# Kernel tuning notes

Hardware: AMD Instinct MI355X
Metric: run time of the kernel (lower is better)

Reference implementation:

```python
import jax, jax.numpy as jnp
import numpy as np

L, EMB, NH, HD, V = 4, 1024, 16, 64, 16000
Q, B, M = 512, 4, 512


def layer_norm(x, g, b, eps=1e-5):
    mu = jnp.mean(x, -1, keepdims=True)
    var = jnp.mean((x - mu) ** 2, -1, keepdims=True)
    return (x - mu) * jax.lax.rsqrt(var + eps) * g + b


def rel_shift(x):
    # x: [q, i, b, h] -> Transformer-XL relative shift via zero-pad + reshape
    q, i, bb, h = x.shape
    zp = jnp.zeros((q, 1, bb, h), x.dtype)
    return jnp.concatenate([zp, x], axis=1).reshape(i + 1, q, bb, h)[1:].reshape(q, i, bb, h)


def setup_inputs() -> dict:
    key = jax.random.key(0)
    ks = jax.random.split(key, 12)
    s = 0.02
    return {
        'input_idxs': jax.random.randint(ks[0], (Q, B), 0, V, dtype=jnp.int32),
        'memory': jax.random.normal(ks[1], (L, M, B, EMB), jnp.float32),
        'embedding': jax.random.normal(ks[2], (V, EMB), jnp.float32) * s,
        'proj_b': jnp.zeros((V,), jnp.float32),
        'u_bias': jax.random.normal(ks[3], (NH, HD), jnp.float32) * s,
        'v_bias': jax.random.normal(ks[4], (NH, HD), jnp.float32) * s,
        'Wq': jax.random.normal(ks[5], (L, NH * HD, EMB), jnp.float32) * s,
        'Wkv': jax.random.normal(ks[6], (L, 2 * NH * HD, EMB), jnp.float32) * s,
        'Wp': jax.random.normal(ks[7], (L, NH * HD, EMB), jnp.float32) * s,
        'fc_w': jax.random.normal(ks[8], (L, EMB, NH * HD), jnp.float32) * s,
        'ff1_w': jax.random.normal(ks[9], (L, 4 * EMB, EMB), jnp.float32) * s,
        'ff1_b': jnp.zeros((L, 4 * EMB), jnp.float32),
        'ff2_w': jax.random.normal(ks[10], (L, EMB, 4 * EMB), jnp.float32) * s,
        'ff2_b': jnp.zeros((L, EMB), jnp.float32),
        'ln_g': jnp.ones((L, EMB), jnp.float32),
        'ln_b': jnp.zeros((L, EMB), jnp.float32),
    }


def reference(input_idxs, memory, embedding, proj_b, u_bias, v_bias, Wq, Wkv, Wp,
              fc_w, ff1_w, ff1_b, ff2_w, ff2_b, ln_g, ln_b):
    # NOTE: faithful to the source, which uses scale = 1 / head_dim**5 (not **0.5)
    scale = 1.0 / (HD ** 5)
    x = embedding[input_idxs] * jnp.asarray(EMB ** 0.5, jnp.float32)  # [Q,B,E]

    # sinusoidal relative positions, descending M+Q-1 .. 0
    pos = jnp.arange(M + Q - 1, -1, -1, dtype=jnp.float32)
    inv_freq = 1.0 / (10000.0 ** (jnp.arange(0, EMB, 2, dtype=jnp.float32) / EMB))
    angle = pos[:, None] * inv_freq[None, :]
    emb_pos = jnp.concatenate([jnp.sin(angle), jnp.cos(angle)], axis=1)  # [M+Q,E]

    mask = jnp.triu(jnp.ones((Q, M + Q), bool), k=1 + M)  # [Q,I]

    for l in range(L):
        e = jnp.concatenate([memory[l], x], axis=0)  # [I,B,E], I = M+Q
        kv = jnp.einsum('ibe,fe->ibf', e, Wkv[l])
        k, v = jnp.split(kv, 2, axis=-1)
        k = k.reshape(M + Q, B, NH, HD)
        v = v.reshape(M + Q, B, NH, HD)
        q = jnp.einsum('qbe,fe->qbf', x, Wq[l]).reshape(Q, B, NH, HD)
        p = (emb_pos @ Wp[l].T).reshape(M + Q, NH, HD)

        att_c = jnp.einsum('qbhd,ibhd->qibh', q + u_bias, k)
        att_p = rel_shift(jnp.einsum('qbhd,ihd->qibh', q + v_bias, p))
        att = att_c + att_p
        att = jnp.where(mask[:, :, None, None], -jnp.inf, att)
        att = jax.nn.softmax(att * scale, axis=1)

        o = jnp.einsum('qibh,ibhd->qbhd', att, v).reshape(Q, B, NH * HD)
        o = o @ fc_w[l].T
        h = layer_norm(o + x, ln_g[l], ln_b[l])
        f = jax.nn.relu(h @ ff1_w[l].T + ff1_b[l]) @ ff2_w[l].T + ff2_b[l]
        x = layer_norm(f + h, ln_g[l], ln_b[l])

    return x @ embedding.T + proj_b  # tied projection, [Q,B,V]
```

## Files before the change

kernel.cpp:

```cpp
#include <hip/hip_runtime.h>


typedef unsigned short u16;
typedef unsigned int u32;
typedef __bf16 bf16x8 __attribute__((ext_vector_type(8)));
typedef float f32x4 __attribute__((ext_vector_type(4)));

#define AS1 __attribute__((address_space(1)))
#define AS3 __attribute__((address_space(3)))

__device__ __forceinline__ u16 f2bf(float f) {
  u32 u = __float_as_uint(f);
  u32 r = (u + 0x7FFFu + ((u >> 16) & 1u)) >> 16;
  return (u16)r;
}
__device__ __forceinline__ float bf2f(u16 u) {
  return __uint_as_float(((u32)u) << 16);
}

struct alignas(8) us4 { u16 x, y, z, w; };

__global__ void k_conv(const float* __restrict__ src, u16* __restrict__ dst, int n4) {
  int i = blockIdx.x * blockDim.x + threadIdx.x;
  int stride = gridDim.x * blockDim.x;
  const float4* s4 = (const float4*)src;
  us4* d4 = (us4*)dst;
  for (; i < n4; i += stride) {
    float4 v = s4[i];
    us4 o; o.x = f2bf(v.x); o.y = f2bf(v.y); o.z = f2bf(v.z); o.w = f2bf(v.w);
    d4[i] = o;
  }
}

__global__ void k_embed(const int* __restrict__ idx, const float* __restrict__ emb,
                        float* __restrict__ x, u16* __restrict__ xb) {
  int r = blockIdx.x, t = threadIdx.x;
  int id = idx[r];
  float4 v = ((const float4*)(emb + (size_t)id * 1024))[t];
  v.x *= 32.0f; v.y *= 32.0f; v.z *= 32.0f; v.w *= 32.0f;
  ((float4*)(x + (size_t)r * 1024))[t] = v;
  us4 o; o.x = f2bf(v.x); o.y = f2bf(v.y); o.z = f2bf(v.z); o.w = f2bf(v.w);
  ((us4*)(xb + (size_t)r * 1024))[t] = o;
}

__global__ void k_ln(const float* __restrict__ a, const float* __restrict__ res,
                     const float* __restrict__ g, const float* __restrict__ bb,
                     float* __restrict__ outf, u16* __restrict__ outb) {
  int r = blockIdx.x, t = threadIdx.x;
  float4 va = ((const float4*)(a + (size_t)r * 1024))[t];
  float4 vr = ((const float4*)(res + (size_t)r * 1024))[t];
  float y0 = va.x + vr.x, y1 = va.y + vr.y, y2 = va.z + vr.z, y3 = va.w + vr.w;
  float s = y0 + y1 + y2 + y3;
  float sq = y0 * y0 + y1 * y1 + y2 * y2 + y3 * y3;
  for (int o = 32; o > 0; o >>= 1) { s += __shfl_xor(s, o); sq += __shfl_xor(sq, o); }
  __shared__ float ls[8];
  int w = t >> 6;
  if ((t & 63) == 0) { ls[w * 2] = s; ls[w * 2 + 1] = sq; }
  __syncthreads();
  s = ls[0] + ls[2] + ls[4] + ls[6];
  sq = ls[1] + ls[3] + ls[5] + ls[7];
  float mu = s * (1.0f / 1024.0f);
  float var = sq * (1.0f / 1024.0f) - mu * mu;
  float rs = rsqrtf(var + 1e-5f);
  float4 vg = ((const float4*)g)[t];
  float4 vb = ((const float4*)bb)[t];
  float o0 = (y0 - mu) * rs * vg.x + vb.x;
  float o1 = (y1 - mu) * rs * vg.y + vb.y;
  float o2v = (y2 - mu) * rs * vg.z + vb.z;
  float o3 = (y3 - mu) * rs * vg.w + vb.w;
  float4 of; of.x = o0; of.y = o1; of.z = o2v; of.w = o3;
  ((float4*)(outf + (size_t)r * 1024))[t] = of;
  us4 oo; oo.x = f2bf(o0); oo.y = f2bf(o1); oo.z = f2bf(o2v); oo.w = f2bf(o3);
  ((us4*)(outb + (size_t)r * 1024))[t] = oo;
}

__global__ void k_psum(const u16* __restrict__ v, float* __restrict__ part) {
  int bx = blockIdx.x;
  int c = bx >> 4, b = (bx >> 2) & 3, fg = bx & 3;
  int f = fg * 256 + threadIdx.x;
  float s = 0.f;
  for (int j = 0; j < 64; j++) {
    int i = c * 64 + j;
    s += bf2f(v[((size_t)(i * 4 + b)) * 1024 + f]);
  }
  part[(size_t)(c * 4 + b) * 1024 + f] = s;
}

__global__ void k_pmean(const u16* __restrict__ v, const float* __restrict__ part,
                        u16* __restrict__ ob) {
  int bx = blockIdx.x;
  int qc = bx >> 4, b = (bx >> 2) & 3, fg = bx & 3;
  int f = fg * 256 + threadIdx.x;
  float run = 0.f;
  int cend = 8 + qc;
  for (int c = 0; c < cend; c++) run += part[(size_t)(c * 4 + b) * 1024 + f];
  for (int j = 0; j < 64; j++) {
    int i = 512 + qc * 64 + j;
    run += bf2f(v[((size_t)(i * 4 + b)) * 1024 + f]);
    ob[((size_t)((i - 512) * 4 + b)) * 1024 + f] = f2bf(run / (float)(i + 1));
  }
}

template <int BIAS, int RELU, int OUTBF>
__global__ __launch_bounds__(256, 2) void k_gemm(
    const u16* __restrict__ A, const u16* __restrict__ A2, int split,
    const u16* __restrict__ B, float* __restrict__ Cf, u16* __restrict__ Cb,
    const float* __restrict__ bias, int M, int N, int K) {
  __shared__ __align__(16) u16 As[128 * 64];
  __shared__ __align__(16) u16 Bs[128 * 64];
  const int tid = threadIdx.x;
  const int lane = tid & 63, wid = tid >> 6;
  const int la = lane & 15, lb = lane >> 4;
  const int row0 = blockIdx.x * 128, col0 = blockIdx.y * 128;
  const int wm = wid >> 1, wn = wid & 1;
  const size_t Kb = (size_t)K * 2;
  const u16* Au = A; int arow = row0;
  if (row0 >= split) { Au = A2; arow = row0 - split; }
  const char* Ab = (const char*)Au + (size_t)arow * Kb;
  const char* Bb = (const char*)B + (size_t)col0 * Kb;
  f32x4 acc[4][4] = {};
  for (int k0 = 0; k0 < K; k0 += 64) {
#pragma unroll
    for (int s = 0; s < 4; s++) {
      int off = s * 4096 + tid * 16;
      int rr = off >> 7, cb = off & 127;
      __builtin_amdgcn_global_load_lds(
          (AS1 void*)(Ab + (size_t)rr * Kb + (size_t)(k0 * 2 + cb)),
          (AS3 void*)((char*)As + s * 4096 + wid * 1024), 16, 0, 0);
    }
#pragma unroll
    for (int s = 0; s < 4; s++) {
      int off = s * 4096 + tid * 16;
      int rr = off >> 7, cb = off & 127;
      __builtin_amdgcn_global_load_lds(
          (AS1 void*)(Bb + (size_t)rr * Kb + (size_t)(k0 * 2 + cb)),
          (AS3 void*)((char*)Bs + s * 4096 + wid * 1024), 16, 0, 0);
    }
    __syncthreads();
    bf16x8 af[2][4], bfv[2][4];
#pragma unroll
    for (int kk = 0; kk < 2; kk++) {
#pragma unroll
      for (int i = 0; i < 4; i++) {
        af[kk][i] = *reinterpret_cast<const bf16x8*>(
            &As[(wm * 64 + i * 16 + la) * 64 + kk * 32 + lb * 8]);
        bfv[kk][i] = *reinterpret_cast<const bf16x8*>(
            &Bs[(wn * 64 + i * 16 + la) * 64 + kk * 32 + lb * 8]);
      }
    }
#pragma unroll
    for (int kk = 0; kk < 2; kk++)
#pragma unroll
      for (int mi = 0; mi < 4; mi++)
#pragma unroll
        for (int ni = 0; ni < 4; ni++)
          acc[mi][ni] = __builtin_amdgcn_mfma_f32_16x16x32_bf16(
              af[kk][mi], bfv[kk][ni], acc[mi][ni], 0, 0, 0);
    __syncthreads();
  }
#pragma unroll
  for (int ni = 0; ni < 4; ni++) {
    int c = col0 + wn * 64 + ni * 16 + la;
    float bv = 0.f;
    if (BIAS) bv = bias[c];
#pragma unroll
    for (int mi = 0; mi < 4; mi++) {
#pragma unroll
      for (int j = 0; j < 4; j++) {
        int rr = row0 + wm * 64 + mi * 16 + lb * 4 + j;
        float vv = acc[mi][ni][j];
        if (BIAS) vv += bv;
        if (RELU) vv = fmaxf(vv, 0.f);
        if (OUTBF) Cb[(size_t)rr * N + c] = f2bf(vv);
        else       Cf[(size_t)rr * N + c] = vv;
      }
    }
  }
}

extern "C" void kernel_launch(void* const* d_in, const int* in_sizes, int n_in,
                              void* d_out, int out_size, void* d_ws, size_t ws_size,
                              hipStream_t stream) {
  const int* idxs = (const int*)d_in[0];
  const float* memory = (const float*)d_in[1];
  const float* embedding = (const float*)d_in[2];
  const float* proj_b = (const float*)d_in[3];
  const float* Wkv = (const float*)d_in[7];
  const float* fc_w = (const float*)d_in[9];
  const float* ff1_w = (const float*)d_in[10];
  const float* ff1_b = (const float*)d_in[11];
  const float* ff2_w = (const float*)d_in[12];
  const float* ff2_b = (const float*)d_in[13];
  const float* ln_g = (const float*)d_in[14];
  const float* ln_b = (const float*)d_in[15];
  float* out = (float*)d_out;

  float* ws = (float*)d_ws;
  float* x    = ws + 0;
  float* h    = ws + 2097152;
  float* o2   = ws + 4194304;
  u16* xb     = (u16*)(ws + 6291456);
  u16* hb     = (u16*)(ws + 7340032);
  u16* ob     = (u16*)(ws + 8388608);
  float* part = ws + 9437184;
  u16* wvv    = (u16*)(ws + 9502720);
  u16* wfc    = (u16*)(ws + 10027008);
  u16* wf1    = (u16*)(ws + 10551296);
  u16* wf2    = (u16*)(ws + 12648448);
  float* big  = ws + 14745600;
  u16* vbuf   = (u16*)(big);
  u16* memb   = (u16*)(big + 2097152);
  u16* f1     = (u16*)(big + 3145728);
  u16* embb   = (u16*)(big);

  auto conv = [&](const float* s, u16* d, int n) {
    int n4 = n >> 2;
    int blocks = (n4 + 255) / 256; if (blocks > 4096) blocks = 4096;
    k_conv<<<blocks, 256, 0, stream>>>(s, d, n4);
  };

  const int BIG = 1 << 30;
  k_embed<<<2048, 256, 0, stream>>>(idxs, embedding, x, xb);

  for (int l = 0; l < 4; l++) {
    conv(Wkv + (size_t)l * 2097152 + 1048576, wvv, 1048576);
    conv(fc_w + (size_t)l * 1048576, wfc, 1048576);
    conv(ff1_w + (size_t)l * 4194304, wf1, 4194304);
    conv(ff2_w + (size_t)l * 4194304, wf2, 4194304);
    conv(memory + (size_t)l * 2097152, memb, 2097152);

    k_gemm<0, 0, 1><<<dim3(32, 8), 256, 0, stream>>>(
        memb, xb, 2048, wvv, nullptr, vbuf, nullptr, 4096, 1024, 1024);

    k_psum<<<256, 256, 0, stream>>>(vbuf, part);
    k_pmean<<<128, 256, 0, stream>>>(vbuf, part, ob);

    k_gemm<0, 0, 0><<<dim3(16, 8), 256, 0, stream>>>(
        ob, ob, BIG, wfc, o2, nullptr, nullptr, 2048, 1024, 1024);
    k_ln<<<2048, 256, 0, stream>>>(o2, x, ln_g + l * 1024, ln_b + l * 1024, h, hb);
    k_gemm<1, 1, 1><<<dim3(16, 32), 256, 0, stream>>>(
        hb, hb, BIG, wf1, nullptr, f1, ff1_b + l * 4096, 2048, 4096, 1024);
    k_gemm<1, 0, 0><<<dim3(16, 8), 256, 0, stream>>>(
        f1, f1, BIG, wf2, o2, nullptr, ff2_b + l * 1024, 2048, 1024, 4096);
    k_ln<<<2048, 256, 0, stream>>>(o2, h, ln_g + l * 1024, ln_b + l * 1024, x, xb);
  }

  conv(embedding, embb, 16384000);
  k_gemm<1, 0, 0><<<dim3(16, 125), 256, 0, stream>>>(
      xb, xb, BIG, embb, out, nullptr, proj_b, 2048, 16000, 1024);
}
```

Before: 1.204 ms.

## Add BM=64 GEMM tiles, XCD-aware block remap, fused conv, vectorized prefix mean

The GEMM kernel gets a template for 64-row tiles, used for the small-N GEMMs so more workgroups fill the GPU. It also remaps workgroup IDs so that neighbouring tiles land on the same XCD for L2 reuse. The five per-layer weight and memory conversions are merged into one launch, and the prefix-sum and prefix-mean kernels now use 4-wide vector loads with fewer blocks. The risks are less reuse per tile with the smaller BM, and lower parallelism in the psum/pmean kernels.

```diff
diff --git a/kernel.cpp b/kernel.cpp
--- a/kernel.cpp
+++ b/kernel.cpp
@@ -29,6 +29,28 @@
     float4 v = s4[i];
     us4 o; o.x = f2bf(v.x); o.y = f2bf(v.y); o.z = f2bf(v.z); o.w = f2bf(v.w);
     d4[i] = o;
+  }
+}
+
+__global__ void k_conv5(const float* __restrict__ s0, u16* __restrict__ d0,
+                        const float* __restrict__ s1, u16* __restrict__ d1,
+                        const float* __restrict__ s2, u16* __restrict__ d2,
+                        const float* __restrict__ s3, u16* __restrict__ d3,
+                        const float* __restrict__ s4, u16* __restrict__ d4) {
+  const int n0 = 262144, n1 = 262144, n2 = 1048576, n3 = 1048576;
+  const int total = 3145728;
+  int i = blockIdx.x * 256 + threadIdx.x;
+  int stride = gridDim.x * 256;
+  for (; i < total; i += stride) {
+    const float* s; u16* d; int j = i;
+    if (j < n0) { s = s0; d = d0; }
+    else if ((j -= n0) < n1) { s = s1; d = d1; }
+    else if ((j -= n1) < n2) { s = s2; d = d2; }
+    else if ((j -= n2) < n3) { s = s3; d = d3; }
+    else { j -= n3; s = s4; d = d4; }
+    float4 v = ((const float4*)s)[j];
+    us4 o; o.x = f2bf(v.x); o.y = f2bf(v.y); o.z = f2bf(v.z); o.w = f2bf(v.w);
+    ((us4*)d)[j] = o;
   }
 }
 
@@ -76,52 +98,75 @@
 
 __global__ void k_psum(const u16* __restrict__ v, float* __restrict__ part) {
   int bx = blockIdx.x;
-  int c = bx >> 4, b = (bx >> 2) & 3, fg = bx & 3;
-  int f = fg * 256 + threadIdx.x;
-  float s = 0.f;
+  int c = bx >> 2, b = bx & 3;
+  int f4 = threadIdx.x;
+  float4 s = {0.f, 0.f, 0.f, 0.f};
   for (int j = 0; j < 64; j++) {
     int i = c * 64 + j;
-    s += bf2f(v[((size_t)(i * 4 + b)) * 1024 + f]);
-  }
-  part[(size_t)(c * 4 + b) * 1024 + f] = s;
+    us4 u = ((const us4*)(v + (size_t)(i * 4 + b) * 1024))[f4];
+    s.x += bf2f(u.x); s.y += bf2f(u.y); s.z += bf2f(u.z); s.w += bf2f(u.w);
+  }
+  ((float4*)(part + (size_t)(c * 4 + b) * 1024))[f4] = s;
 }
 
 __global__ void k_pmean(const u16* __restrict__ v, const float* __restrict__ part,
                         u16* __restrict__ ob) {
   int bx = blockIdx.x;
-  int qc = bx >> 4, b = (bx >> 2) & 3, fg = bx & 3;
-  int f = fg * 256 + threadIdx.x;
-  float run = 0.f;
+  int qc = bx >> 2, b = bx & 3;
+  int f4 = threadIdx.x;
+  float4 run = {0.f, 0.f, 0.f, 0.f};
   int cend = 8 + qc;
-  for (int c = 0; c < cend; c++) run += part[(size_t)(c * 4 + b) * 1024 + f];
+  for (int cc = 0; cc < cend; cc++) {
+    float4 p = ((const float4*)(part + (size_t)(cc * 4 + b) * 1024))[f4];
+    run.x += p.x; run.y += p.y; run.z += p.z; run.w += p.w;
+  }
   for (int j = 0; j < 64; j++) {
     int i = 512 + qc * 64 + j;
-    run += bf2f(v[((size_t)(i * 4 + b)) * 1024 + f]);
-    ob[((size_t)((i - 512) * 4 + b)) * 1024 + f] = f2bf(run / (float)(i + 1));
-  }
-}
-
-template <int BIAS, int RELU, int OUTBF>
+    us4 u = ((const us4*)(v + (size_t)(i * 4 + b) * 1024))[f4];
+    run.x += bf2f(u.x); run.y += bf2f(u.y); run.z += bf2f(u.z); run.w += bf2f(u.w);
+    float inv = 1.0f / (float)(i + 1);
+    us4 o; o.x = f2bf(run.x * inv); o.y = f2bf(run.y * inv);
+    o.z = f2bf(run.z * inv); o.w = f2bf(run.w * inv);
+    ((us4*)(ob + (size_t)((i - 512) * 4 + b) * 1024))[f4] = o;
+  }
+}
+
+template <int BM, int BIAS, int RELU, int OUTBF>
 __global__ __launch_bounds__(256, 2) void k_gemm(
     const u16* __restrict__ A, const u16* __restrict__ A2, int split,
     const u16* __restrict__ B, float* __restrict__ Cf, u16* __restrict__ Cb,
     const float* __restrict__ bias, int M, int N, int K) {
-  __shared__ __align__(16) u16 As[128 * 64];
+  constexpr int SA = BM / 32;
+  constexpr int NI = (BM == 128) ? 4 : 2;
+  __shared__ __align__(16) u16 As[BM * 64];
   __shared__ __align__(16) u16 Bs[128 * 64];
   const int tid = threadIdx.x;
   const int lane = tid & 63, wid = tid >> 6;
   const int la = lane & 15, lb = lane >> 4;
-  const int row0 = blockIdx.x * 128, col0 = blockIdx.y * 128;
-  const int wm = wid >> 1, wn = wid & 1;
+  int bx = blockIdx.x, by = blockIdx.y;
+  {
+    int gx = gridDim.x;
+    int nwg = gx * gridDim.y;
+    int orig = by * gx + bx;
+    int q = nwg >> 3, r = nwg & 7;
+    int xcd = orig & 7, j = orig >> 3;
+    int wg = (xcd < r ? xcd * (q + 1) : r * (q + 1) + (xcd - r) * q) + j;
+    bx = wg % gx; by = wg / gx;
+  }
+  const int row0 = bx * BM, col0 = by * 128;
+  const int wm = (BM == 128) ? (wid >> 1) : 0;
+  const int wn = (BM == 128) ? (wid & 1) : wid;
+  const int mbase = wm * 64;
+  const int nbase = (BM == 128) ? wn * 64 : wn * 32;
   const size_t Kb = (size_t)K * 2;
   const u16* Au = A; int arow = row0;
   if (row0 >= split) { Au = A2; arow = row0 - split; }
   const char* Ab = (const char*)Au + (size_t)arow * Kb;
   const char* Bb = (const char*)B + (size_t)col0 * Kb;
-  f32x4 acc[4][4] = {};
+  f32x4 acc[4][NI] = {};
   for (int k0 = 0; k0 < K; k0 += 64) {
 #pragma unroll
-    for (int s = 0; s < 4; s++) {
+    for (int s = 0; s < SA; s++) {
       int off = s * 4096 + tid * 16;
       int rr = off >> 7, cb = off & 127;
       __builtin_amdgcn_global_load_lds(
@@ -137,37 +182,38 @@
           (AS3 void*)((char*)Bs + s * 4096 + wid * 1024), 16, 0, 0);
     }
     __syncthreads();
-    bf16x8 af[2][4], bfv[2][4];
+    bf16x8 af[2][4], bfv[2][NI];
 #pragma unroll
     for (int kk = 0; kk < 2; kk++) {
 #pragma unroll
-      for (int i = 0; i < 4; i++) {
+      for (int i = 0; i < 4; i++)
         af[kk][i] = *reinterpret_cast<const bf16x8*>(
-            &As[(wm * 64 + i * 16 + la) * 64 + kk * 32 + lb * 8]);
+            &As[(mbase + i * 16 + la) * 64 + kk * 32 + lb * 8]);
+#pragma unroll
+      for (int i = 0; i < NI; i++)
         bfv[kk][i] = *reinterpret_cast<const bf16x8*>(
-            &Bs[(wn * 64 + i * 16 + la) * 64 + kk * 32 + lb * 8]);
-      }
+            &Bs[(nbase + i * 16 + la) * 64 + kk * 32 + lb * 8]);
     }
 #pragma unroll
     for (int kk = 0; kk < 2; kk++)
 #pragma unroll
       for (int mi = 0; mi < 4; mi++)
 #pragma unroll
-        for (int ni = 0; ni < 4; ni++)
+        for (int ni = 0; ni < NI; ni++)
           acc[mi][ni] = __builtin_amdgcn_mfma_f32_16x16x32_bf16(
               af[kk][mi], bfv[kk][ni], acc[mi][ni], 0, 0, 0);
     __syncthreads();
   }
 #pragma unroll
-  for (int ni = 0; ni < 4; ni++) {
-    int c = col0 + wn * 64 + ni * 16 + la;
+  for (int ni = 0; ni < NI; ni++) {
+    int c = col0 + nbase + ni * 16 + la;
     float bv = 0.f;
     if (BIAS) bv = bias[c];
 #pragma unroll
     for (int mi = 0; mi < 4; mi++) {
 #pragma unroll
       for (int j = 0; j < 4; j++) {
-        int rr = row0 + wm * 64 + mi * 16 + lb * 4 + j;
+        int rr = row0 + mbase + mi * 16 + lb * 4 + j;
         float vv = acc[mi][ni][j];
         if (BIAS) vv += bv;
         if (RELU) vv = fmaxf(vv, 0.f);
@@ -213,39 +259,37 @@
   u16* f1     = (u16*)(big + 3145728);
   u16* embb   = (u16*)(big);
 
-  auto conv = [&](const float* s, u16* d, int n) {
-    int n4 = n >> 2;
-    int blocks = (n4 + 255) / 256; if (blocks > 4096) blocks = 4096;
-    k_conv<<<blocks, 256, 0, stream>>>(s, d, n4);
-  };
-
   const int BIG = 1 << 30;
   k_embed<<<2048, 256, 0, stream>>>(idxs, embedding, x, xb);
 
   for (int l = 0; l < 4; l++) {
-    conv(Wkv + (size_t)l * 2097152 + 1048576, wvv, 1048576);
-    conv(fc_w + (size_t)l * 1048576, wfc, 1048576);
-    conv(ff1_w + (size_t)l * 4194304, wf1, 4194304);
-    conv(ff2_w + (size_t)l * 4194304, wf2, 4194304);
-    conv(memory + (size_t)l * 2097152, memb, 2097152);
-
-    k_gemm<0, 0, 1><<<dim3(32, 8), 256, 0, stream>>>(
+    k_conv5<<<2048, 256, 0, stream>>>(
+        Wkv + (size_t)l * 2097152 + 1048576, wvv,
+        fc_w + (size_t)l * 1048576, wfc,
+        ff1_w + (size_t)l * 4194304, wf1,
+        ff2_w + (size_t)l * 4194304, wf2,
+        memory + (size_t)l * 2097152, memb);
+
+    k_gemm<64, 0, 0, 1><<<dim3(64, 8), 256, 0, stream>>>(
         memb, xb, 2048, wvv, nullptr, vbuf, nullptr, 4096, 1024, 1024);
 
-    k_psum<<<256, 256, 0, stream>>>(vbuf, part);
-    k_pmean<<<128, 256, 0, stream>>>(vbuf, part, ob);
-
-    k_gemm<0, 0, 0><<<dim3(16, 8), 256, 0, stream>>>(
+    k_psum<<<64, 256, 0, stream>>>(vbuf, part);
+    k_pmean<<<32, 256, 0, stream>>>(vbuf, part, ob);
+
+    k_gemm<64, 0, 0, 0><<<dim3(32, 8), 256, 0, stream>>>(
         ob, ob, BIG, wfc, o2, nullptr, nullptr, 2048, 1024, 1024);
     k_ln<<<2048, 256, 0, stream>>>(o2, x, ln_g + l * 1024, ln_b + l * 1024, h, hb);
-    k_gemm<1, 1, 1><<<dim3(16, 32), 256, 0, stream>>>(
+    k_gemm<128, 1, 1, 1><<<dim3(16, 32), 256, 0, stream>>>(
         hb, hb, BIG, wf1, nullptr, f1, ff1_b + l * 4096, 2048, 4096, 1024);
-    k_gemm<1, 0, 0><<<dim3(16, 8), 256, 0, stream>>>(
+    k_gemm<64, 1, 0, 0><<<dim3(32, 8), 256, 0, stream>>>(
         f1, f1, BIG, wf2, o2, nullptr, ff2_b + l * 1024, 2048, 1024, 4096);
     k_ln<<<2048, 256, 0, stream>>>(o2, h, ln_g + l * 1024, ln_b + l * 1024, x, xb);
   }
 
-  conv(embedding, embb, 16384000);
-  k_gemm<1, 0, 0><<<dim3(16, 125), 256, 0, stream>>>(
+  {
+    int n4 = 16384000 >> 2;
+    k_conv<<<4096, 256, 0, stream>>>(embedding, embb, n4);
+  }
+  k_gemm<128, 1, 0, 0><<<dim3(16, 125), 256, 0, stream>>>(
       xb, xb, BIG, embb, out, nullptr, proj_b, 2048, 16000, 1024);
 }
```

Result: faster. 1.130 ms (-6.1%).
